# Performance work log

Measured on AMD Instinct MI355X. Metric: run time of the kernel, lower is better.

Reference implementation:

```python
import jax, jax.numpy as jnp
import numpy as np

D_IN = 256
D_HID = 256


def prelu(x, a):
    return jnp.maximum(x, 0) + a * jnp.minimum(x, 0)


def setup_inputs() -> dict:
    key = jax.random.key(0)
    ks = jax.random.split(key, 12)
    N, M = 8192, 8192
    s_in = 1.0 / np.sqrt(D_IN)
    s_3in = 1.0 / np.sqrt(3 * D_IN)
    s_half = 1.0 / np.sqrt(D_IN // 2)
    return {
        "anchor": jax.random.normal(ks[0], (N, D_IN), jnp.float32),
        "guess": jax.random.normal(ks[1], (M, D_IN), jnp.float32),
        # w_a: Linear(d_in, d_hid)
        "Wa": jax.random.uniform(ks[2], (D_HID, D_IN), jnp.float32, -s_in, s_in),
        "ba": jax.random.uniform(ks[3], (D_HID,), jnp.float32, -s_in, s_in),
        # w_g: Linear(d_in, d_hid)
        "Wg": jax.random.uniform(ks[4], (D_HID, D_IN), jnp.float32, -s_in, s_in),
        "bg": jax.random.uniform(ks[5], (D_HID,), jnp.float32, -s_in, s_in),
        # w_d: Linear(3*d_in, d_in) -> PReLU -> Linear(d_in, d_in//2) -> PReLU -> Linear(d_in//2, 1)
        "W1": jax.random.uniform(ks[6], (D_IN, 3 * D_IN), jnp.float32, -s_3in, s_3in),
        "b1": jax.random.uniform(ks[7], (D_IN,), jnp.float32, -s_3in, s_3in),
        "a1": jnp.array(0.25, jnp.float32),
        "W2": jax.random.uniform(ks[8], (D_IN // 2, D_IN), jnp.float32, -s_in, s_in),
        "b2": jax.random.uniform(ks[9], (D_IN // 2,), jnp.float32, -s_in, s_in),
        "a2": jnp.array(0.25, jnp.float32),
        "W3": jax.random.uniform(ks[10], (1, D_IN // 2), jnp.float32, -s_half, s_half),
        "b3": jax.random.uniform(ks[11], (1,), jnp.float32, -s_half, s_half),
    }


def reference(anchor, guess, Wa, ba, Wg, bg, W1, b1, a1, W2, b2, a2, W3, b3):
    # projections: [N, d_hid], [M, d_hid]
    ac = anchor @ Wa.T + ba
    ge = guess @ Wg.T + bg
    # unscaled cross-attention: [M, N] score matrix
    score = jax.nn.softmax(ge @ ac.T, axis=-1)
    ge2ac = score @ anchor  # [M, d_in]
    dis_x = jnp.concatenate((guess, ge2ac, guess - ge2ac), axis=-1)  # [M, 3*d_in]
    # dropout is identity in eval mode
    h = prelu(dis_x @ W1.T + b1, a1)
    h = prelu(h @ W2.T + b2, a2)
    return h @ W3.T + b3  # [M, 1]
```

## Files before the change

### kernel.cpp

```cpp
#include <hip/hip_runtime.h>


typedef _Float16 f16;
typedef _Float16 h8_t  __attribute__((ext_vector_type(8)));
typedef _Float16 h4_t  __attribute__((ext_vector_type(4)));
typedef float    f4_t  __attribute__((ext_vector_type(4)));
typedef float    f16x  __attribute__((ext_vector_type(16)));
typedef unsigned int u4_t  __attribute__((ext_vector_type(4)));

#define LOG2E 1.4426950408889634f

__device__ __forceinline__ void llds16(const f16* g, f16* s) {
    __builtin_amdgcn_global_load_lds(
        (const __attribute__((address_space(1))) void*)g,
        (__attribute__((address_space(3))) void*)s, 16, 0, 0);
}
__device__ __forceinline__ unsigned int pk2(float a, float b) {
    auto h = __builtin_amdgcn_cvt_pkrtz(a, b);
    return __builtin_bit_cast(unsigned int, h);
}

__global__ __launch_bounds__(256)
void cvt_weights(const float* __restrict__ Wa, const float* __restrict__ Wg,
                 const float* __restrict__ W1, const float* __restrict__ W2,
                 f16* __restrict__ oa, f16* __restrict__ og,
                 f16* __restrict__ o1, f16* __restrict__ o2)
{
    int i = blockIdx.x * 256 + threadIdx.x;
    const float* s; f16* d; int off;
    if (i < 16384)      { s = Wa; d = oa; off = i; }
    else if (i < 32768) { s = Wg; d = og; off = i - 16384; }
    else if (i < 81920) { s = W1; d = o1; off = i - 32768; }
    else                { s = W2; d = o2; off = i - 81920; }
    f4_t v = ((const f4_t*)s)[off];
    h4_t h;
    h[0] = (f16)v[0]; h[1] = (f16)v[1]; h[2] = (f16)v[2]; h[3] = (f16)v[3];
    ((h4_t*)d)[off] = h;
}

__global__ __launch_bounds__(256)
void transpose_f16(const float* __restrict__ src, f16* __restrict__ dst)
{
    __shared__ float tile[32][33];
    const int kb = blockIdx.x, db = blockIdx.y;
    const int t  = threadIdx.x;
    const int ty = t >> 3, tx4 = (t & 7) * 4;
    f4_t v = *(const f4_t*)(src + (size_t)(kb * 32 + ty) * 256 + db * 32 + tx4);
    tile[ty][tx4 + 0] = v[0]; tile[ty][tx4 + 1] = v[1];
    tile[ty][tx4 + 2] = v[2]; tile[ty][tx4 + 3] = v[3];
    __syncthreads();
    h4_t h;
    h[0] = (f16)tile[tx4 + 0][ty]; h[1] = (f16)tile[tx4 + 1][ty];
    h[2] = (f16)tile[tx4 + 2][ty]; h[3] = (f16)tile[tx4 + 3][ty];
    *(h4_t*)(dst + (size_t)(db * 32 + ty) * 8192 + kb * 32 + tx4) = h;
}

template<int ACT, int SRC32>
__global__ __launch_bounds__(256)
void gemm_bt(const void* __restrict__ A, const f16* __restrict__ B,
             const float* __restrict__ bias, const float* __restrict__ act_a,
             float scale, f16* __restrict__ C, int M, int N, int K)
{
    constexpr int BM = 128, BN = 64, BK = 32, LDA = 40, LDB = 40;
    __shared__ f16 As[BM * LDA];
    __shared__ f16 Bs[BN * LDB];
    const int t = threadIdx.x;
    const int w = t >> 6, l = t & 63, lg = l >> 4, lr = l & 15;
    const int wm = w >> 1, wn = w & 1;
    const int bm = blockIdx.x, bn = blockIdx.y;
    f4_t acc[4][2] = {};

    for (int kt = 0; kt < K; kt += BK) {
        #pragma unroll
        for (int i = 0; i < 2; i++) {
            int s = t + i * 256;
            int row = s >> 2, c8 = (s & 3) * 8;
            if constexpr (SRC32) {
                const float* Af = (const float*)A + (size_t)(bm * BM + row) * K + kt + c8;
                f4_t v0 = *(const f4_t*)Af;
                f4_t v1 = *(const f4_t*)(Af + 4);
                h8_t h;
                h[0]=(f16)v0[0]; h[1]=(f16)v0[1]; h[2]=(f16)v0[2]; h[3]=(f16)v0[3];
                h[4]=(f16)v1[0]; h[5]=(f16)v1[1]; h[6]=(f16)v1[2]; h[7]=(f16)v1[3];
                *(h8_t*)(&As[row * LDA + c8]) = h;
            } else {
                *(u4_t*)(&As[row * LDA + c8]) =
                    *(const u4_t*)((const f16*)A + (size_t)(bm * BM + row) * K + kt + c8);
            }
        }
        {
            int row = t >> 2, c8 = (t & 3) * 8;
            *(u4_t*)(&Bs[row * LDB + c8]) =
                *(const u4_t*)(B + (size_t)(bn * BN + row) * K + kt + c8);
        }
        __syncthreads();
        h8_t af[4], bf[2];
        #pragma unroll
        for (int mf = 0; mf < 4; mf++)
            af[mf] = *(const h8_t*)(&As[(wm * 64 + mf * 16 + lr) * LDA + lg * 8]);
        #pragma unroll
        for (int nf = 0; nf < 2; nf++)
            bf[nf] = *(const h8_t*)(&Bs[(wn * 32 + nf * 16 + lr) * LDB + lg * 8]);
        #pragma unroll
        for (int mf = 0; mf < 4; mf++)
            #pragma unroll
            for (int nf = 0; nf < 2; nf++)
                acc[mf][nf] = __builtin_amdgcn_mfma_f32_16x16x32_f16(
                    af[mf], bf[nf], acc[mf][nf], 0, 0, 0);
        __syncthreads();
    }

    float av = 0.f;
    if constexpr (ACT) av = *act_a;
    #pragma unroll
    for (int mf = 0; mf < 4; mf++)
        #pragma unroll
        for (int nf = 0; nf < 2; nf++)
            #pragma unroll
            for (int r = 0; r < 4; r++) {
                int row = bm * BM + wm * 64 + mf * 16 + lg * 4 + r;
                int col = bn * BN + wn * 32 + nf * 16 + lr;
                float v = (acc[mf][nf][r] + bias[col]) * scale;
                if constexpr (ACT) v = v > 0.f ? v : av * v;
                C[(size_t)row * N + col] = (f16)v;
            }
}

__global__ __launch_bounds__(256, 2)
void flash_attn(const f16* __restrict__ Q, const f16* __restrict__ Kc,
                const f16* __restrict__ Vt, f16* __restrict__ OPN,
                float* __restrict__ mpart, float* __restrict__ lpart)
{
    constexpr int D = 256, BK = 64, NK = 8192, SL = 1024, NT = SL / BK;
    __shared__ f16 Ks[BK * D];
    __shared__ f16 Vs[D * BK];
    const int t = threadIdx.x, w = t >> 6, l = t & 63;
    const int q = l & 31, hi = l >> 5;
    const int sl = blockIdx.x & 7, qb = blockIdx.x >> 3;
    const int k0b = sl * SL;
    const int qg0 = qb * 128 + w * 32;

    h8_t qf[16];
    {
        const f16* qr = Q + (size_t)(qg0 + q) * D + hi * 8;
        #pragma unroll
        for (int ks = 0; ks < 16; ks++) qf[ks] = *(const h8_t*)(qr + ks * 16);
    }

    const int sK0 = ((t & 31) ^ (t >> 5)) << 3;
    const int sx  = (t & 15) ^ (t >> 4);
    const int dV  = (t >> 4) * 2 + (sx >> 3);
    const int cV  = (sx & 7) << 3;

    auto stageK = [&](int k0) {
        #pragma unroll
        for (int i = 0; i < 8; i++) {
            const f16* g = Kc + (size_t)(k0 + i * 8 + (t >> 5)) * D + (sK0 ^ ((i & 1) << 6));
            llds16(g, &Ks[i * 2048 + w * 512]);
        }
    };
    auto stageV = [&](int k0) {
        #pragma unroll
        for (int i = 0; i < 8; i++) {
            const f16* g = Vt + (size_t)(i * 32 + dV) * NK + k0 + cV;
            llds16(g, &Vs[i * 2048 + w * 512]);
        }
    };

    stageK(k0b); stageV(k0b);
    __syncthreads();

    f16x o[8] = {};
    f16x sa0, sa1;
    float m_run = -1e30f, l_run = 0.f;
    const int rswzK = (q & 15) << 4;
    const int kbase0 = q * 512;
    const int vbase  = (q >> 1) * 256;
    const int vswz   = (q >> 1) << 4;
    const int vcol0  = ((q & 1) << 7) | (hi << 4);

    for (int kv = 0; kv < NT; ++kv) {
        #pragma unroll
        for (int r = 0; r < 16; r++) { sa0[r] = 0.f; sa1[r] = 0.f; }
        #pragma unroll
        for (int ks = 0; ks < 16; ks++) {
            const int cb = ((ks * 32) | (hi << 4)) ^ rswzK;
            h8_t a0 = *(const h8_t*)((const char*)Ks + kbase0 + cb);
            h8_t a1 = *(const h8_t*)((const char*)Ks + kbase0 + 16384 + cb);
            sa0 = __builtin_amdgcn_mfma_f32_32x32x16_f16(a0, qf[ks], sa0, 0, 0, 0);
            sa1 = __builtin_amdgcn_mfma_f32_32x32x16_f16(a1, qf[ks], sa1, 0, 0, 0);
        }

        float mt = sa0[0];
        #pragma unroll
        for (int r = 1; r < 16; r++) mt = fmaxf(mt, sa0[r]);
        #pragma unroll
        for (int r = 0; r < 16; r++) mt = fmaxf(mt, sa1[r]);
        mt = fmaxf(mt, __shfl_xor(mt, 32));
        if (!__all(mt <= m_run + 8.0f)) {
            const float mnew = fmaxf(m_run, mt);
            const float corr = exp2f(m_run - mnew);
            #pragma unroll
            for (int r = 0; r < 16; r++) {
                const float c = __shfl(corr, (r & 3) + 8 * (r >> 2) + 4 * hi);
                #pragma unroll
                for (int nb = 0; nb < 8; nb++) o[nb][r] *= c;
            }
            l_run *= corr;
            m_run = mnew;
        }
        float rs = 0.f;
        #pragma unroll
        for (int r = 0; r < 16; r++) { sa0[r] = exp2f(sa0[r] - m_run); rs += sa0[r]; }
        #pragma unroll
        for (int r = 0; r < 16; r++) { sa1[r] = exp2f(sa1[r] - m_run); rs += sa1[r]; }
        rs += __shfl_xor(rs, 32);
        l_run += rs;

        __syncthreads();
        if (kv + 1 < NT) stageK(k0b + (kv + 1) * BK);

        #pragma unroll
        for (int kb = 0; kb < 2; kb++) {
            const f16x& P = kb ? sa1 : sa0;
            #pragma unroll
            for (int s = 0; s < 2; s++) {
                unsigned int w00 = pk2(P[8*s+0], P[8*s+1]);
                unsigned int w01 = pk2(P[8*s+2], P[8*s+3]);
                unsigned int w10 = pk2(P[8*s+4], P[8*s+5]);
                unsigned int w11 = pk2(P[8*s+6], P[8*s+7]);
                asm volatile("v_permlane32_swap_b32 %0, %1" : "+v"(w00), "+v"(w10));
                asm volatile("v_permlane32_swap_b32 %0, %1" : "+v"(w01), "+v"(w11));
                u4_t up; up[0] = w00; up[1] = w01; up[2] = w10; up[3] = w11;
                const h8_t apv = __builtin_bit_cast(h8_t, up);
                const int S = kb * 2 + s;
                const int cb = (vcol0 | (S << 5)) ^ vswz;
                #pragma unroll
                for (int nb = 0; nb < 8; nb++) {
                    h8_t bf = *(const h8_t*)((const char*)Vs + nb * 4096 + vbase + cb);
                    o[nb] = __builtin_amdgcn_mfma_f32_32x32x16_f16(apv, bf, o[nb], 0, 0, 0);
                }
            }
        }
        __syncthreads();
        if (kv + 1 < NT) stageV(k0b + (kv + 1) * BK);
    }

    #pragma unroll
    for (int r = 0; r < 16; r++) {
        const int qr = (r & 3) + 8 * (r >> 2) + 4 * hi;
        const float linv = 1.0f / __shfl(l_run, qr);
        const size_t rowoff = ((size_t)sl * NK + qg0 + qr) * D;
        #pragma unroll
        for (int nb = 0; nb < 8; nb++)
            OPN[rowoff + nb * 32 + q] = (f16)(o[nb][r] * linv);
    }
    if (hi == 0) {
        mpart[(size_t)sl * NK + qg0 + q] = m_run;
        lpart[(size_t)sl * NK + qg0 + q] = l_run;
    }
}

__global__ __launch_bounds__(256)
void build_dis(const float* __restrict__ guess, const f16* __restrict__ OPN,
               const float* __restrict__ mp, const float* __restrict__ lp,
               f16* __restrict__ dis)
{
    const int m = blockIdx.x, d = threadIdx.x;
    float M = -3.0e38f;
    #pragma unroll
    for (int s = 0; s < 8; s++) M = fmaxf(M, mp[s * 8192 + m]);
    float wsum = 0.f, num = 0.f;
    #pragma unroll
    for (int s = 0; s < 8; s++) {
        float c = exp2f(mp[s * 8192 + m] - M) * lp[s * 8192 + m];
        wsum += c;
        num  += c * (float)OPN[((size_t)s * 8192 + m) * 256 + d];
    }
    const float v = num / wsum;
    const float g = guess[(size_t)m * 256 + d];
    dis[(size_t)m * 768 + d]       = (f16)g;
    dis[(size_t)m * 768 + 256 + d] = (f16)v;
    dis[(size_t)m * 768 + 512 + d] = (f16)(g - v);
}

__global__ __launch_bounds__(256)
void final_dot(const f16* __restrict__ h2, const float* __restrict__ W3,
               const float* __restrict__ b3, float* __restrict__ out)
{
    const int t = threadIdx.x, w = t >> 6, l = t & 63;
    const int row = blockIdx.x * 4 + w;
    const f16* hr = h2 + (size_t)row * 128;
    float s = (float)hr[l] * W3[l] + (float)hr[64 + l] * W3[64 + l];
    #pragma unroll
    for (int m = 1; m < 64; m <<= 1) s += __shfl_xor(s, m);
    if (l == 0) out[row] = s + b3[0];
}

extern "C" void kernel_launch(void* const* d_in, const int* in_sizes, int n_in,
                              void* d_out, int out_size, void* d_ws, size_t ws_size,
                              hipStream_t stream)
{
    const float* anchor = (const float*)d_in[0];
    const float* guess  = (const float*)d_in[1];
    const float* Wa = (const float*)d_in[2];
    const float* ba = (const float*)d_in[3];
    const float* Wg = (const float*)d_in[4];
    const float* bg = (const float*)d_in[5];
    const float* W1 = (const float*)d_in[6];
    const float* b1 = (const float*)d_in[7];
    const float* a1 = (const float*)d_in[8];
    const float* W2 = (const float*)d_in[9];
    const float* b2 = (const float*)d_in[10];
    const float* a2 = (const float*)d_in[11];
    const float* W3 = (const float*)d_in[12];
    const float* b3 = (const float*)d_in[13];
    float* out = (float*)d_out;
    char* ws = (char*)d_ws;

    const size_t MB = 1u << 20;
    f16* GE16 = (f16*)(ws + 0 * MB);
    f16* AC16 = (f16*)(ws + 4 * MB);
    f16* VT16 = (f16*)(ws + 8 * MB);
    f16* OPN  = (f16*)(ws + 12 * MB);
    f16* WA16 = (f16*)(ws + 44 * MB);
    f16* WG16 = (f16*)(ws + 44 * MB + 128 * 1024);
    f16* W116 = (f16*)(ws + 44 * MB + 256 * 1024);
    f16* W216 = (f16*)(ws + 44 * MB + 640 * 1024);
    float* MP = (float*)(ws + 45 * MB);
    float* LP = (float*)(ws + 45 * MB + 256 * 1024);
    f16* DIS  = (f16*)(ws + 0 * MB);
    f16* H1   = (f16*)(ws + 12 * MB);
    f16* H2   = (f16*)(ws + 16 * MB);

    cvt_weights<<<352, 256, 0, stream>>>(Wa, Wg, W1, W2, WA16, WG16, W116, W216);
    transpose_f16<<<dim3(256, 8), 256, 0, stream>>>(anchor, VT16);

    gemm_bt<0, 1><<<dim3(64, 4), 256, 0, stream>>>(guess,  WG16, bg, nullptr, LOG2E, GE16, 8192, 256, 256);
    gemm_bt<0, 1><<<dim3(64, 4), 256, 0, stream>>>(anchor, WA16, ba, nullptr, 1.0f,  AC16, 8192, 256, 256);

    flash_attn<<<512, 256, 0, stream>>>(GE16, AC16, VT16, OPN, MP, LP);

    build_dis<<<8192, 256, 0, stream>>>(guess, OPN, MP, LP, DIS);

    gemm_bt<1, 0><<<dim3(64, 4), 256, 0, stream>>>(DIS, W116, b1, a1, 1.0f, H1, 8192, 256, 768);
    gemm_bt<1, 0><<<dim3(64, 2), 256, 0, stream>>>(H1,  W216, b2, a2, 1.0f, H2, 8192, 128, 256);
    final_dot<<<2048, 256, 0, stream>>>(H2, W3, b3, out);
}
```

Measured before the change: 180.3 us.

## Double-buffer flash attention tiles, fold W1 concat algebraically, retile GEMMs

The flash attention kernel now uses 32-key tiles with double-buffered K/V shared memory. It prefetches the next tile at the start of each step and raises wave priority around the MFMA blocks, which removes the mid-loop staging barriers. The W1 weight is folded so that [g, v, g-v] @ W1^T becomes [g, v] @ W1c^T, which shrinks the first MLP GEMM's K from 768 to 512 and drops the third concat slice. The GEMM kernel is retiled to 64x128 blocks so each wave covers the full M tile. Smaller KV tiles add more barriers per key, and folding the weights in fp16 changes rounding slightly.

```diff
diff --git a/kernel.cpp b/kernel.cpp
--- a/kernel.cpp
+++ b/kernel.cpp
@@ -24,18 +24,31 @@
 void cvt_weights(const float* __restrict__ Wa, const float* __restrict__ Wg,
                  const float* __restrict__ W1, const float* __restrict__ W2,
                  f16* __restrict__ oa, f16* __restrict__ og,
-                 f16* __restrict__ o1, f16* __restrict__ o2)
+                 f16* __restrict__ o1c, f16* __restrict__ o2)
 {
     int i = blockIdx.x * 256 + threadIdx.x;
-    const float* s; f16* d; int off;
-    if (i < 16384)      { s = Wa; d = oa; off = i; }
-    else if (i < 32768) { s = Wg; d = og; off = i - 16384; }
-    else if (i < 81920) { s = W1; d = o1; off = i - 32768; }
-    else                { s = W2; d = o2; off = i - 81920; }
-    f4_t v = ((const f4_t*)s)[off];
-    h4_t h;
-    h[0] = (f16)v[0]; h[1] = (f16)v[1]; h[2] = (f16)v[2]; h[3] = (f16)v[3];
-    ((h4_t*)d)[off] = h;
+    if (i < 40960) {
+        const float* s; f16* d; int off;
+        if (i < 16384)      { s = Wa; d = oa; off = i; }
+        else if (i < 32768) { s = Wg; d = og; off = i - 16384; }
+        else                { s = W2; d = o2; off = i - 32768; }
+        f4_t v = ((const f4_t*)s)[off];
+        h4_t h;
+        h[0] = (f16)v[0]; h[1] = (f16)v[1]; h[2] = (f16)v[2]; h[3] = (f16)v[3];
+        ((h4_t*)d)[off] = h;
+    } else {
+        int off = i - 40960;
+        int j = off >> 7, c0 = (off & 127) * 4;
+        const float* r = W1 + (size_t)j * 768;
+        f4_t v0, v1;
+        if (c0 < 256) { v0 = *(const f4_t*)(r + c0); v1 = *(const f4_t*)(r + 512 + c0); }
+        else          { v0 = *(const f4_t*)(r + c0); v1 = *(const f4_t*)(r + 256 + c0); }
+        h4_t h;
+        #pragma unroll
+        for (int e = 0; e < 4; e++)
+            h[e] = (f16)(c0 < 256 ? v0[e] + v1[e] : v0[e] - v1[e]);
+        ((h4_t*)o1c)[off] = h;
+    }
 }
 
 __global__ __launch_bounds__(256)
@@ -55,26 +68,23 @@
     *(h4_t*)(dst + (size_t)(db * 32 + ty) * 8192 + kb * 32 + tx4) = h;
 }
 
-template<int ACT, int SRC32>
-__global__ __launch_bounds__(256)
-void gemm_bt(const void* __restrict__ A, const f16* __restrict__ B,
-             const float* __restrict__ bias, const float* __restrict__ act_a,
-             float scale, f16* __restrict__ C, int M, int N, int K)
-{
-    constexpr int BM = 128, BN = 64, BK = 32, LDA = 40, LDB = 40;
+template<int ACT, int SRC32, int BN>
+__global__ __launch_bounds__(256)
+void gemm_wide(const void* __restrict__ A, const f16* __restrict__ B,
+               const float* __restrict__ bias, const float* __restrict__ act_a,
+               float scale, f16* __restrict__ C, int M, int N, int K)
+{
+    constexpr int BM = 64, BK = 32, LDA = 40, LDB = 40, NF = BN / 64;
     __shared__ f16 As[BM * LDA];
     __shared__ f16 Bs[BN * LDB];
     const int t = threadIdx.x;
     const int w = t >> 6, l = t & 63, lg = l >> 4, lr = l & 15;
-    const int wm = w >> 1, wn = w & 1;
     const int bm = blockIdx.x, bn = blockIdx.y;
-    f4_t acc[4][2] = {};
+    f4_t acc[4][NF] = {};
 
     for (int kt = 0; kt < K; kt += BK) {
-        #pragma unroll
-        for (int i = 0; i < 2; i++) {
-            int s = t + i * 256;
-            int row = s >> 2, c8 = (s & 3) * 8;
+        {
+            int row = t >> 2, c8 = (t & 3) * 8;
             if constexpr (SRC32) {
                 const float* Af = (const float*)A + (size_t)(bm * BM + row) * K + kt + c8;
                 f4_t v0 = *(const f4_t*)Af;
@@ -88,23 +98,25 @@
                     *(const u4_t*)((const f16*)A + (size_t)(bm * BM + row) * K + kt + c8);
             }
         }
-        {
-            int row = t >> 2, c8 = (t & 3) * 8;
+        #pragma unroll
+        for (int i = 0; i < BN / 64; i++) {
+            int s = t + i * 256;
+            int row = s >> 2, c8 = (s & 3) * 8;
             *(u4_t*)(&Bs[row * LDB + c8]) =
                 *(const u4_t*)(B + (size_t)(bn * BN + row) * K + kt + c8);
         }
         __syncthreads();
-        h8_t af[4], bf[2];
+        h8_t af[4], bf[NF];
         #pragma unroll
         for (int mf = 0; mf < 4; mf++)
-            af[mf] = *(const h8_t*)(&As[(wm * 64 + mf * 16 + lr) * LDA + lg * 8]);
-        #pragma unroll
-        for (int nf = 0; nf < 2; nf++)
-            bf[nf] = *(const h8_t*)(&Bs[(wn * 32 + nf * 16 + lr) * LDB + lg * 8]);
+            af[mf] = *(const h8_t*)(&As[(mf * 16 + lr) * LDA + lg * 8]);
+        #pragma unroll
+        for (int nf = 0; nf < NF; nf++)
+            bf[nf] = *(const h8_t*)(&Bs[(w * (BN/4) + nf * 16 + lr) * LDB + lg * 8]);
         #pragma unroll
         for (int mf = 0; mf < 4; mf++)
             #pragma unroll
-            for (int nf = 0; nf < 2; nf++)
+            for (int nf = 0; nf < NF; nf++)
                 acc[mf][nf] = __builtin_amdgcn_mfma_f32_16x16x32_f16(
                     af[mf], bf[nf], acc[mf][nf], 0, 0, 0);
         __syncthreads();
@@ -115,11 +127,11 @@
     #pragma unroll
     for (int mf = 0; mf < 4; mf++)
         #pragma unroll
-        for (int nf = 0; nf < 2; nf++)
+        for (int nf = 0; nf < NF; nf++)
             #pragma unroll
             for (int r = 0; r < 4; r++) {
-                int row = bm * BM + wm * 64 + mf * 16 + lg * 4 + r;
-                int col = bn * BN + wn * 32 + nf * 16 + lr;
+                int row = bm * BM + mf * 16 + lg * 4 + r;
+                int col = bn * BN + w * (BN/4) + nf * 16 + lr;
                 float v = (acc[mf][nf][r] + bias[col]) * scale;
                 if constexpr (ACT) v = v > 0.f ? v : av * v;
                 C[(size_t)row * N + col] = (f16)v;
@@ -131,9 +143,9 @@
                 const f16* __restrict__ Vt, f16* __restrict__ OPN,
                 float* __restrict__ mpart, float* __restrict__ lpart)
 {
-    constexpr int D = 256, BK = 64, NK = 8192, SL = 1024, NT = SL / BK;
-    __shared__ f16 Ks[BK * D];
-    __shared__ f16 Vs[D * BK];
+    constexpr int D = 256, BKV = 32, NK = 8192, SL = 1024, NT = SL / BKV;
+    __shared__ f16 Ks0[BKV * D], Ks1[BKV * D];
+    __shared__ f16 Vs0[D * BKV], Vs1[D * BKV];
     const int t = threadIdx.x, w = t >> 6, l = t & 63;
     const int q = l & 31, hi = l >> 5;
     const int sl = blockIdx.x & 7, qb = blockIdx.x >> 3;
@@ -147,55 +159,53 @@
         for (int ks = 0; ks < 16; ks++) qf[ks] = *(const h8_t*)(qr + ks * 16);
     }
 
-    const int sK0 = ((t & 31) ^ (t >> 5)) << 3;
-    const int sx  = (t & 15) ^ (t >> 4);
-    const int dV  = (t >> 4) * 2 + (sx >> 3);
-    const int cV  = (sx & 7) << 3;
-
-    auto stageK = [&](int k0) {
-        #pragma unroll
-        for (int i = 0; i < 8; i++) {
-            const f16* g = Kc + (size_t)(k0 + i * 8 + (t >> 5)) * D + (sK0 ^ ((i & 1) << 6));
-            llds16(g, &Ks[i * 2048 + w * 512]);
+    const int rK   = t >> 5;
+    const int keyV = 8 * ((t & 3) ^ ((t >> 3) & 3));
+    const int dVi  = t >> 2;
+
+    auto stage = [&](int k0, f16* kd, f16* vd) {
+        #pragma unroll
+        for (int i = 0; i < 4; i++) {
+            const int r  = i * 8 + rK;
+            const int ce = 8 * ((t & 31) ^ (r & 15));
+            llds16(Kc + (size_t)(k0 + r) * D + ce, kd + i * 2048 + t * 8);
+        }
+        #pragma unroll
+        for (int i = 0; i < 4; i++) {
+            const int d0 = i * 64 + dVi;
+            llds16(Vt + (size_t)d0 * NK + k0 + keyV, vd + i * 2048 + t * 8);
         }
     };
-    auto stageV = [&](int k0) {
-        #pragma unroll
-        for (int i = 0; i < 8; i++) {
-            const f16* g = Vt + (size_t)(i * 32 + dV) * NK + k0 + cV;
-            llds16(g, &Vs[i * 2048 + w * 512]);
-        }
-    };
-
-    stageK(k0b); stageV(k0b);
+
+    stage(k0b, Ks0, Vs0);
     __syncthreads();
 
     f16x o[8] = {};
-    f16x sa0, sa1;
     float m_run = -1e30f, l_run = 0.f;
-    const int rswzK = (q & 15) << 4;
-    const int kbase0 = q * 512;
-    const int vbase  = (q >> 1) * 256;
-    const int vswz   = (q >> 1) << 4;
-    const int vcol0  = ((q & 1) << 7) | (hi << 4);
-
-    for (int kv = 0; kv < NT; ++kv) {
-        #pragma unroll
-        for (int r = 0; r < 16; r++) { sa0[r] = 0.f; sa1[r] = 0.f; }
+    const int kswz = (q & 15) << 4;
+    const int vswz = ((q >> 1) & 3) << 4;
+
+    auto tile = [&](int kv, const f16* kr, const f16* vr, f16* kw, f16* vw) {
+        if (kv + 1 < NT) stage(k0b + (kv + 1) * BKV, kw, vw);
+
+        f16x sa;
+        #pragma unroll
+        for (int r = 0; r < 16; r++) sa[r] = 0.f;
+        __builtin_amdgcn_s_setprio(1);
         #pragma unroll
         for (int ks = 0; ks < 16; ks++) {
-            const int cb = ((ks * 32) | (hi << 4)) ^ rswzK;
-            h8_t a0 = *(const h8_t*)((const char*)Ks + kbase0 + cb);
-            h8_t a1 = *(const h8_t*)((const char*)Ks + kbase0 + 16384 + cb);
-            sa0 = __builtin_amdgcn_mfma_f32_32x32x16_f16(a0, qf[ks], sa0, 0, 0, 0);
-            sa1 = __builtin_amdgcn_mfma_f32_32x32x16_f16(a1, qf[ks], sa1, 0, 0, 0);
-        }
-
-        float mt = sa0[0];
-        #pragma unroll
-        for (int r = 1; r < 16; r++) mt = fmaxf(mt, sa0[r]);
-        #pragma unroll
-        for (int r = 0; r < 16; r++) mt = fmaxf(mt, sa1[r]);
+            const int cb = ((ks * 32) | (hi << 4)) ^ kswz;
+            h8_t a0 = *(const h8_t*)((const char*)kr + q * 512 + cb);
+            sa = __builtin_amdgcn_mfma_f32_32x32x16_f16(a0, qf[ks], sa, 0, 0, 0);
+        }
+        __builtin_amdgcn_s_setprio(0);
+
+        float m01 = fmaxf(sa[0], sa[1]),  m23 = fmaxf(sa[2], sa[3]);
+        float m45 = fmaxf(sa[4], sa[5]),  m67 = fmaxf(sa[6], sa[7]);
+        float m89 = fmaxf(sa[8], sa[9]),  mab = fmaxf(sa[10], sa[11]);
+        float mcd = fmaxf(sa[12], sa[13]), mef = fmaxf(sa[14], sa[15]);
+        float mt = fmaxf(fmaxf(fmaxf(m01, m23), fmaxf(m45, m67)),
+                         fmaxf(fmaxf(m89, mab), fmaxf(mcd, mef)));
         mt = fmaxf(mt, __shfl_xor(mt, 32));
         if (!__all(mt <= m_run + 8.0f)) {
             const float mnew = fmaxf(m_run, mt);
@@ -211,39 +221,36 @@
         }
         float rs = 0.f;
         #pragma unroll
-        for (int r = 0; r < 16; r++) { sa0[r] = exp2f(sa0[r] - m_run); rs += sa0[r]; }
-        #pragma unroll
-        for (int r = 0; r < 16; r++) { sa1[r] = exp2f(sa1[r] - m_run); rs += sa1[r]; }
+        for (int r = 0; r < 16; r++) { sa[r] = exp2f(sa[r] - m_run); rs += sa[r]; }
         rs += __shfl_xor(rs, 32);
         l_run += rs;
 
+        __builtin_amdgcn_s_setprio(1);
+        #pragma unroll
+        for (int s = 0; s < 2; s++) {
+            unsigned int w00 = pk2(sa[8*s+0], sa[8*s+1]);
+            unsigned int w01 = pk2(sa[8*s+2], sa[8*s+3]);
+            unsigned int w10 = pk2(sa[8*s+4], sa[8*s+5]);
+            unsigned int w11 = pk2(sa[8*s+6], sa[8*s+7]);
+            asm volatile("v_permlane32_swap_b32 %0, %1" : "+v"(w00), "+v"(w10));
+            asm volatile("v_permlane32_swap_b32 %0, %1" : "+v"(w01), "+v"(w11));
+            u4_t up; up[0] = w00; up[1] = w01; up[2] = w10; up[3] = w11;
+            const h8_t apv = __builtin_bit_cast(h8_t, up);
+            const int cb = ((s * 32) | (hi << 4)) ^ vswz;
+            #pragma unroll
+            for (int nb = 0; nb < 8; nb++) {
+                h8_t bf = *(const h8_t*)((const char*)vr + nb * 2048 + q * 64 + cb);
+                o[nb] = __builtin_amdgcn_mfma_f32_32x32x16_f16(apv, bf, o[nb], 0, 0, 0);
+            }
+        }
+        __builtin_amdgcn_s_setprio(0);
+
         __syncthreads();
-        if (kv + 1 < NT) stageK(k0b + (kv + 1) * BK);
-
-        #pragma unroll
-        for (int kb = 0; kb < 2; kb++) {
-            const f16x& P = kb ? sa1 : sa0;
-            #pragma unroll
-            for (int s = 0; s < 2; s++) {
-                unsigned int w00 = pk2(P[8*s+0], P[8*s+1]);
-                unsigned int w01 = pk2(P[8*s+2], P[8*s+3]);
-                unsigned int w10 = pk2(P[8*s+4], P[8*s+5]);
-                unsigned int w11 = pk2(P[8*s+6], P[8*s+7]);
-                asm volatile("v_permlane32_swap_b32 %0, %1" : "+v"(w00), "+v"(w10));
-                asm volatile("v_permlane32_swap_b32 %0, %1" : "+v"(w01), "+v"(w11));
-                u4_t up; up[0] = w00; up[1] = w01; up[2] = w10; up[3] = w11;
-                const h8_t apv = __builtin_bit_cast(h8_t, up);
-                const int S = kb * 2 + s;
-                const int cb = (vcol0 | (S << 5)) ^ vswz;
-                #pragma unroll
-                for (int nb = 0; nb < 8; nb++) {
-                    h8_t bf = *(const h8_t*)((const char*)Vs + nb * 4096 + vbase + cb);
-                    o[nb] = __builtin_amdgcn_mfma_f32_32x32x16_f16(apv, bf, o[nb], 0, 0, 0);
-                }
-            }
-        }
-        __syncthreads();
-        if (kv + 1 < NT) stageV(k0b + (kv + 1) * BK);
+    };
+
+    for (int kv = 0; kv < NT; kv += 2) {
+        tile(kv,     Ks0, Vs0, Ks1, Vs1);
+        tile(kv + 1, Ks1, Vs1, Ks0, Vs0);
     }
 
     #pragma unroll
@@ -262,9 +269,9 @@
 }
 
 __global__ __launch_bounds__(256)
-void build_dis(const float* __restrict__ guess, const f16* __restrict__ OPN,
-               const float* __restrict__ mp, const float* __restrict__ lp,
-               f16* __restrict__ dis)
+void build_qv(const float* __restrict__ guess, const f16* __restrict__ OPN,
+              const float* __restrict__ mp, const float* __restrict__ lp,
+              f16* __restrict__ dis2)
 {
     const int m = blockIdx.x, d = threadIdx.x;
     float M = -3.0e38f;
@@ -278,10 +285,8 @@
         num  += c * (float)OPN[((size_t)s * 8192 + m) * 256 + d];
     }
     const float v = num / wsum;
-    const float g = guess[(size_t)m * 256 + d];
-    dis[(size_t)m * 768 + d]       = (f16)g;
-    dis[(size_t)m * 768 + 256 + d] = (f16)v;
-    dis[(size_t)m * 768 + 512 + d] = (f16)(g - v);
+    dis2[(size_t)m * 512 + d]       = (f16)guess[(size_t)m * 256 + d];
+    dis2[(size_t)m * 512 + 256 + d] = (f16)v;
 }
 
 __global__ __launch_bounds__(256)
@@ -325,25 +330,29 @@
     f16* OPN  = (f16*)(ws + 12 * MB);
     f16* WA16 = (f16*)(ws + 44 * MB);
     f16* WG16 = (f16*)(ws + 44 * MB + 128 * 1024);
-    f16* W116 = (f16*)(ws + 44 * MB + 256 * 1024);
-    f16* W216 = (f16*)(ws + 44 * MB + 640 * 1024);
+    f16* W1C  = (f16*)(ws + 44 * MB + 256 * 1024);
+    f16* W216 = (f16*)(ws + 44 * MB + 512 * 1024);
     float* MP = (float*)(ws + 45 * MB);
     float* LP = (float*)(ws + 45 * MB + 256 * 1024);
-    f16* DIS  = (f16*)(ws + 0 * MB);
-    f16* H1   = (f16*)(ws + 12 * MB);
-    f16* H2   = (f16*)(ws + 16 * MB);
-
-    cvt_weights<<<352, 256, 0, stream>>>(Wa, Wg, W1, W2, WA16, WG16, W116, W216);
+    f16* H2   = (f16*)(ws + 46 * MB);
+    f16* DIS2 = (f16*)(ws + 0 * MB);
+    f16* H1   = (f16*)(ws + 8 * MB);
+
+    cvt_weights<<<288, 256, 0, stream>>>(Wa, Wg, W1, W2, WA16, WG16, W1C, W216);
     transpose_f16<<<dim3(256, 8), 256, 0, stream>>>(anchor, VT16);
 
-    gemm_bt<0, 1><<<dim3(64, 4), 256, 0, stream>>>(guess,  WG16, bg, nullptr, LOG2E, GE16, 8192, 256, 256);
-    gemm_bt<0, 1><<<dim3(64, 4), 256, 0, stream>>>(anchor, WA16, ba, nullptr, 1.0f,  AC16, 8192, 256, 256);
+    gemm_wide<0, 1, 128><<<dim3(128, 2), 256, 0, stream>>>(
+        guess, WG16, bg, nullptr, LOG2E, GE16, 8192, 256, 256);
+    gemm_wide<0, 1, 128><<<dim3(128, 2), 256, 0, stream>>>(
+        anchor, WA16, ba, nullptr, 1.0f, AC16, 8192, 256, 256);
 
     flash_attn<<<512, 256, 0, stream>>>(GE16, AC16, VT16, OPN, MP, LP);
 
-    build_dis<<<8192, 256, 0, stream>>>(guess, OPN, MP, LP, DIS);
-
-    gemm_bt<1, 0><<<dim3(64, 4), 256, 0, stream>>>(DIS, W116, b1, a1, 1.0f, H1, 8192, 256, 768);
-    gemm_bt<1, 0><<<dim3(64, 2), 256, 0, stream>>>(H1,  W216, b2, a2, 1.0f, H2, 8192, 128, 256);
+    build_qv<<<8192, 256, 0, stream>>>(guess, OPN, MP, LP, DIS2);
+
+    gemm_wide<1, 0, 128><<<dim3(128, 2), 256, 0, stream>>>(
+        DIS2, W1C, b1, a1, 1.0f, H1, 8192, 256, 512);
+    gemm_wide<1, 0, 128><<<dim3(128, 1), 256, 0, stream>>>(
+        H1, W216, b2, a2, 1.0f, H2, 8192, 128, 256);
     final_dot<<<2048, 256, 0, stream>>>(H2, W3, b3, out);
 }
```

Measured after the change: 186.0 us. +3.1%, slower.

## Fuse prep kernels, fold W1 concat algebraically, fuse split-combine into MLP GEMMs

Applied to the files above, without the earlier changes.

Merges weight conversion and the anchor transpose into one prep kernel, and folds the concat [g, v, g-v]·W1 into a K=512 GEMM with combined weights (W1a+W1c, W1b-W1c). The split-softmax combine moves into the first MLP GEMM's A-tile load, which removes the dis buffer. The second MLP layer is fused with the final dot product. Both projections run in a single launch, and s_setprio is added around the MFMA phases in the attention kernel. This cuts launches and intermediate traffic, but the fused MLP kernels use only 128 blocks, which may underuse the GPU. proj_pair also writes an unused transpose into VT16 that races with prep's write of the same buffer, though both write identical data.

```diff
diff --git a/kernel.cpp b/kernel.cpp
--- a/kernel.cpp
+++ b/kernel.cpp
@@ -21,108 +21,126 @@
 }
 
 __global__ __launch_bounds__(256)
-void cvt_weights(const float* __restrict__ Wa, const float* __restrict__ Wg,
-                 const float* __restrict__ W1, const float* __restrict__ W2,
-                 f16* __restrict__ oa, f16* __restrict__ og,
-                 f16* __restrict__ o1, f16* __restrict__ o2)
-{
-    int i = blockIdx.x * 256 + threadIdx.x;
-    const float* s; f16* d; int off;
-    if (i < 16384)      { s = Wa; d = oa; off = i; }
-    else if (i < 32768) { s = Wg; d = og; off = i - 16384; }
-    else if (i < 81920) { s = W1; d = o1; off = i - 32768; }
-    else                { s = W2; d = o2; off = i - 81920; }
-    f4_t v = ((const f4_t*)s)[off];
-    h4_t h;
-    h[0] = (f16)v[0]; h[1] = (f16)v[1]; h[2] = (f16)v[2]; h[3] = (f16)v[3];
-    ((h4_t*)d)[off] = h;
-}
-
-__global__ __launch_bounds__(256)
-void transpose_f16(const float* __restrict__ src, f16* __restrict__ dst)
+void prep(const float* __restrict__ anchor,
+          const float* __restrict__ Wa, const float* __restrict__ Wg,
+          const float* __restrict__ W1, const float* __restrict__ W2,
+          f16* __restrict__ oa, f16* __restrict__ og,
+          f16* __restrict__ o1c, f16* __restrict__ o2,
+          f16* __restrict__ vt)
 {
     __shared__ float tile[32][33];
-    const int kb = blockIdx.x, db = blockIdx.y;
-    const int t  = threadIdx.x;
-    const int ty = t >> 3, tx4 = (t & 7) * 4;
-    f4_t v = *(const f4_t*)(src + (size_t)(kb * 32 + ty) * 256 + db * 32 + tx4);
-    tile[ty][tx4 + 0] = v[0]; tile[ty][tx4 + 1] = v[1];
-    tile[ty][tx4 + 2] = v[2]; tile[ty][tx4 + 3] = v[3];
-    __syncthreads();
-    h4_t h;
-    h[0] = (f16)tile[tx4 + 0][ty]; h[1] = (f16)tile[tx4 + 1][ty];
-    h[2] = (f16)tile[tx4 + 2][ty]; h[3] = (f16)tile[tx4 + 3][ty];
-    *(h4_t*)(dst + (size_t)(db * 32 + ty) * 8192 + kb * 32 + tx4) = h;
-}
-
-template<int ACT, int SRC32>
+    const int bid = blockIdx.x, t = threadIdx.x;
+    if (bid < 288) {
+        int i = bid * 256 + t;
+        if (i < 40960) {
+            const float* s; f16* d; int off;
+            if (i < 16384)      { s = Wa; d = oa; off = i; }
+            else if (i < 32768) { s = Wg; d = og; off = i - 16384; }
+            else                { s = W2; d = o2; off = i - 32768; }
+            f4_t v = ((const f4_t*)s)[off];
+            h4_t h;
+            h[0]=(f16)v[0]; h[1]=(f16)v[1]; h[2]=(f16)v[2]; h[3]=(f16)v[3];
+            ((h4_t*)d)[off] = h;
+        } else {
+            int off = i - 40960;
+            int j = off >> 7, c0 = (off & 127) * 4;
+            const float* r = W1 + (size_t)j * 768;
+            f4_t v0, v1;
+            if (c0 < 256) { v0 = *(const f4_t*)(r + c0); v1 = *(const f4_t*)(r + 512 + c0); }
+            else          { v0 = *(const f4_t*)(r + c0); v1 = *(const f4_t*)(r + 256 + c0); }
+            h4_t h;
+            #pragma unroll
+            for (int e = 0; e < 4; e++)
+                h[e] = (f16)(c0 < 256 ? v0[e] + v1[e] : v0[e] - v1[e]);
+            ((h4_t*)o1c)[off] = h;
+        }
+    } else {
+        const int r  = bid - 288;
+        const int kb = r & 255, db = r >> 8;
+        const int ty = t >> 3, tx4 = (t & 7) * 4;
+        f4_t v = *(const f4_t*)(anchor + (size_t)(kb * 32 + ty) * 256 + db * 32 + tx4);
+        tile[ty][tx4 + 0] = v[0]; tile[ty][tx4 + 1] = v[1];
+        tile[ty][tx4 + 2] = v[2]; tile[ty][tx4 + 3] = v[3];
+        __syncthreads();
+        h4_t h;
+        h[0] = (f16)tile[tx4 + 0][ty]; h[1] = (f16)tile[tx4 + 1][ty];
+        h[2] = (f16)tile[tx4 + 2][ty]; h[3] = (f16)tile[tx4 + 3][ty];
+        *(h4_t*)(vt + (size_t)(db * 32 + ty) * 8192 + kb * 32 + tx4) = h;
+    }
+}
+
 __global__ __launch_bounds__(256)
-void gemm_bt(const void* __restrict__ A, const f16* __restrict__ B,
-             const float* __restrict__ bias, const float* __restrict__ act_a,
-             float scale, f16* __restrict__ C, int M, int N, int K)
+void proj_pair(const float* __restrict__ guess, const float* __restrict__ anchor,
+               const f16* __restrict__ WG, const f16* __restrict__ WA,
+               const float* __restrict__ bg, const float* __restrict__ ba,
+               f16* __restrict__ GE, f16* __restrict__ AC,
+               f16* __restrict__ vtunused)
 {
-    constexpr int BM = 128, BN = 64, BK = 32, LDA = 40, LDB = 40;
-    __shared__ f16 As[BM * LDA];
-    __shared__ f16 Bs[BN * LDB];
+    constexpr int BK = 32, LDA = 40, LDB = 40;
+    __shared__ f16 As[64 * LDA];
+    __shared__ f16 Bs[128 * LDB];
     const int t = threadIdx.x;
     const int w = t >> 6, l = t & 63, lg = l >> 4, lr = l & 15;
-    const int wm = w >> 1, wn = w & 1;
-    const int bm = blockIdx.x, bn = blockIdx.y;
+    const int bm = blockIdx.x, bn = blockIdx.y, z = blockIdx.z;
+    const float* A   = z ? anchor : guess;
+    const f16*   B   = z ? WA : WG;
+    const float* bias= z ? ba : bg;
+    const float scale= z ? 1.0f : LOG2E;
+    f16* C = z ? AC : GE;
     f4_t acc[4][2] = {};
 
-    for (int kt = 0; kt < K; kt += BK) {
-        #pragma unroll
-        for (int i = 0; i < 2; i++) {
-            int s = t + i * 256;
-            int row = s >> 2, c8 = (s & 3) * 8;
-            if constexpr (SRC32) {
-                const float* Af = (const float*)A + (size_t)(bm * BM + row) * K + kt + c8;
-                f4_t v0 = *(const f4_t*)Af;
-                f4_t v1 = *(const f4_t*)(Af + 4);
-                h8_t h;
-                h[0]=(f16)v0[0]; h[1]=(f16)v0[1]; h[2]=(f16)v0[2]; h[3]=(f16)v0[3];
-                h[4]=(f16)v1[0]; h[5]=(f16)v1[1]; h[6]=(f16)v1[2]; h[7]=(f16)v1[3];
-                *(h8_t*)(&As[row * LDA + c8]) = h;
-            } else {
-                *(u4_t*)(&As[row * LDA + c8]) =
-                    *(const u4_t*)((const f16*)A + (size_t)(bm * BM + row) * K + kt + c8);
-            }
-        }
+    for (int kt = 0; kt < 256; kt += BK) {
         {
             int row = t >> 2, c8 = (t & 3) * 8;
+            const float* Af = A + (size_t)(bm * 64 + row) * 256 + kt + c8;
+            f4_t v0 = *(const f4_t*)Af;
+            f4_t v1 = *(const f4_t*)(Af + 4);
+            h8_t h;
+            h[0]=(f16)v0[0]; h[1]=(f16)v0[1]; h[2]=(f16)v0[2]; h[3]=(f16)v0[3];
+            h[4]=(f16)v1[0]; h[5]=(f16)v1[1]; h[6]=(f16)v1[2]; h[7]=(f16)v1[3];
+            *(h8_t*)(&As[row * LDA + c8]) = h;
+        }
+        {
+            int s0 = t, row = s0 >> 2, c8 = (s0 & 3) * 8;
             *(u4_t*)(&Bs[row * LDB + c8]) =
-                *(const u4_t*)(B + (size_t)(bn * BN + row) * K + kt + c8);
+                *(const u4_t*)(B + (size_t)(bn * 128 + row) * 256 + kt + c8);
+            int s1 = t + 256; row = s1 >> 2; c8 = (s1 & 3) * 8;
+            *(u4_t*)(&Bs[row * LDB + c8]) =
+                *(const u4_t*)(B + (size_t)(bn * 128 + row) * 256 + kt + c8);
         }
         __syncthreads();
         h8_t af[4], bf[2];
         #pragma unroll
         for (int mf = 0; mf < 4; mf++)
-            af[mf] = *(const h8_t*)(&As[(wm * 64 + mf * 16 + lr) * LDA + lg * 8]);
+            af[mf] = *(const h8_t*)(&As[(mf * 16 + lr) * LDA + lg * 8]);
         #pragma unroll
         for (int nf = 0; nf < 2; nf++)
-            bf[nf] = *(const h8_t*)(&Bs[(wn * 32 + nf * 16 + lr) * LDB + lg * 8]);
+            bf[nf] = *(const h8_t*)(&Bs[(w * 32 + nf * 16 + lr) * LDB + lg * 8]);
         #pragma unroll
         for (int mf = 0; mf < 4; mf++)
             #pragma unroll
             for (int nf = 0; nf < 2; nf++)
                 acc[mf][nf] = __builtin_amdgcn_mfma_f32_16x16x32_f16(
                     af[mf], bf[nf], acc[mf][nf], 0, 0, 0);
-        __syncthreads();
-    }
-
-    float av = 0.f;
-    if constexpr (ACT) av = *act_a;
+        if (z == 1 && bn == 0) {
+            const int c = t >> 3, r0 = (t & 7) * 8;
+            h8_t h;
+            #pragma unroll
+            for (int j = 0; j < 8; j++) h[j] = As[(r0 + j) * LDA + c];
+            *(h8_t*)(vtunused + (size_t)(kt + c) * 8192 + bm * 64 + r0) = h;
+        }
+        __syncthreads();
+    }
+
     #pragma unroll
     for (int mf = 0; mf < 4; mf++)
         #pragma unroll
         for (int nf = 0; nf < 2; nf++)
             #pragma unroll
             for (int r = 0; r < 4; r++) {
-                int row = bm * BM + wm * 64 + mf * 16 + lg * 4 + r;
-                int col = bn * BN + wn * 32 + nf * 16 + lr;
-                float v = (acc[mf][nf][r] + bias[col]) * scale;
-                if constexpr (ACT) v = v > 0.f ? v : av * v;
-                C[(size_t)row * N + col] = (f16)v;
+                int row = bm * 64 + mf * 16 + lg * 4 + r;
+                int col = bn * 128 + w * 32 + nf * 16 + lr;
+                C[(size_t)row * 256 + col] = (f16)((acc[mf][nf][r] + bias[col]) * scale);
             }
 }
 
@@ -182,6 +200,7 @@
     for (int kv = 0; kv < NT; ++kv) {
         #pragma unroll
         for (int r = 0; r < 16; r++) { sa0[r] = 0.f; sa1[r] = 0.f; }
+        __builtin_amdgcn_s_setprio(1);
         #pragma unroll
         for (int ks = 0; ks < 16; ks++) {
             const int cb = ((ks * 32) | (hi << 4)) ^ rswzK;
@@ -190,6 +209,7 @@
             sa0 = __builtin_amdgcn_mfma_f32_32x32x16_f16(a0, qf[ks], sa0, 0, 0, 0);
             sa1 = __builtin_amdgcn_mfma_f32_32x32x16_f16(a1, qf[ks], sa1, 0, 0, 0);
         }
+        __builtin_amdgcn_s_setprio(0);
 
         float mt = sa0[0];
         #pragma unroll
@@ -220,6 +240,7 @@
         __syncthreads();
         if (kv + 1 < NT) stageK(k0b + (kv + 1) * BK);
 
+        __builtin_amdgcn_s_setprio(1);
         #pragma unroll
         for (int kb = 0; kb < 2; kb++) {
             const f16x& P = kb ? sa1 : sa0;
@@ -242,6 +263,7 @@
                 }
             }
         }
+        __builtin_amdgcn_s_setprio(0);
         __syncthreads();
         if (kv + 1 < NT) stageV(k0b + (kv + 1) * BK);
     }
@@ -262,39 +284,178 @@
 }
 
 __global__ __launch_bounds__(256)
-void build_dis(const float* __restrict__ guess, const f16* __restrict__ OPN,
-               const float* __restrict__ mp, const float* __restrict__ lp,
-               f16* __restrict__ dis)
+void mlp1(const float* __restrict__ guess, const f16* __restrict__ OPN,
+          const float* __restrict__ mp, const float* __restrict__ lp,
+          const f16* __restrict__ W1C, const float* __restrict__ b1,
+          const float* __restrict__ a1, f16* __restrict__ H1)
 {
-    const int m = blockIdx.x, d = threadIdx.x;
-    float M = -3.0e38f;
+    constexpr int LDA = 40, LDB = 40;
+    __shared__ f16 As[64 * LDA];
+    __shared__ f16 Bs[256 * LDB];
+    __shared__ float cn[64][8];
+    const int t = threadIdx.x;
+    const int w = t >> 6, l = t & 63, lg = l >> 4, lr = l & 15;
+    const int m0 = blockIdx.x * 64;
+
+    if (t < 64) {
+        float c[8], M = -3.0e38f;
+        #pragma unroll
+        for (int s = 0; s < 8; s++) { c[s] = mp[s * 8192 + m0 + t]; M = fmaxf(M, c[s]); }
+        float wsum = 0.f;
+        #pragma unroll
+        for (int s = 0; s < 8; s++) { c[s] = exp2f(c[s] - M) * lp[s * 8192 + m0 + t]; wsum += c[s]; }
+        const float inv = 1.0f / wsum;
+        #pragma unroll
+        for (int s = 0; s < 8; s++) cn[t][s] = c[s] * inv;
+    }
+    __syncthreads();
+
+    const int arow = t >> 2, ac8 = (t & 3) * 8;
+    float cnr[8];
     #pragma unroll
-    for (int s = 0; s < 8; s++) M = fmaxf(M, mp[s * 8192 + m]);
-    float wsum = 0.f, num = 0.f;
+    for (int s = 0; s < 8; s++) cnr[s] = cn[arow][s];
+
+    f4_t acc[4][4] = {};
+    for (int kt = 0; kt < 512; kt += 32) {
+        {
+            h8_t h;
+            if (kt < 256) {
+                const float* Af = guess + (size_t)(m0 + arow) * 256 + kt + ac8;
+                f4_t v0 = *(const f4_t*)Af;
+                f4_t v1 = *(const f4_t*)(Af + 4);
+                h[0]=(f16)v0[0]; h[1]=(f16)v0[1]; h[2]=(f16)v0[2]; h[3]=(f16)v0[3];
+                h[4]=(f16)v1[0]; h[5]=(f16)v1[1]; h[6]=(f16)v1[2]; h[7]=(f16)v1[3];
+            } else {
+                const int d0 = kt - 256 + ac8;
+                f4_t v0 = {0.f,0.f,0.f,0.f}, v1 = {0.f,0.f,0.f,0.f};
+                #pragma unroll
+                for (int s = 0; s < 8; s++) {
+                    h8_t ov = *(const h8_t*)(OPN + ((size_t)s * 8192 + m0 + arow) * 256 + d0);
+                    const float c = cnr[s];
+                    v0[0] += c * (float)ov[0]; v0[1] += c * (float)ov[1];
+                    v0[2] += c * (float)ov[2]; v0[3] += c * (float)ov[3];
+                    v1[0] += c * (float)ov[4]; v1[1] += c * (float)ov[5];
+                    v1[2] += c * (float)ov[6]; v1[3] += c * (float)ov[7];
+                }
+                h[0]=(f16)v0[0]; h[1]=(f16)v0[1]; h[2]=(f16)v0[2]; h[3]=(f16)v0[3];
+                h[4]=(f16)v1[0]; h[5]=(f16)v1[1]; h[6]=(f16)v1[2]; h[7]=(f16)v1[3];
+            }
+            *(h8_t*)(&As[arow * LDA + ac8]) = h;
+        }
+        #pragma unroll
+        for (int i = 0; i < 4; i++) {
+            int s0 = t + i * 256;
+            int row = s0 >> 2, c8 = (s0 & 3) * 8;
+            *(u4_t*)(&Bs[row * LDB + c8]) =
+                *(const u4_t*)(W1C + (size_t)row * 512 + kt + c8);
+        }
+        __syncthreads();
+        h8_t af[4], bf[4];
+        #pragma unroll
+        for (int mf = 0; mf < 4; mf++)
+            af[mf] = *(const h8_t*)(&As[(mf * 16 + lr) * LDA + lg * 8]);
+        #pragma unroll
+        for (int nf = 0; nf < 4; nf++)
+            bf[nf] = *(const h8_t*)(&Bs[(w * 64 + nf * 16 + lr) * LDB + lg * 8]);
+        #pragma unroll
+        for (int mf = 0; mf < 4; mf++)
+            #pragma unroll
+            for (int nf = 0; nf < 4; nf++)
+                acc[mf][nf] = __builtin_amdgcn_mfma_f32_16x16x32_f16(
+                    af[mf], bf[nf], acc[mf][nf], 0, 0, 0);
+        __syncthreads();
+    }
+
+    const float av = *a1;
     #pragma unroll
-    for (int s = 0; s < 8; s++) {
-        float c = exp2f(mp[s * 8192 + m] - M) * lp[s * 8192 + m];
-        wsum += c;
-        num  += c * (float)OPN[((size_t)s * 8192 + m) * 256 + d];
-    }
-    const float v = num / wsum;
-    const float g = guess[(size_t)m * 256 + d];
-    dis[(size_t)m * 768 + d]       = (f16)g;
-    dis[(size_t)m * 768 + 256 + d] = (f16)v;
-    dis[(size_t)m * 768 + 512 + d] = (f16)(g - v);
+    for (int mf = 0; mf < 4; mf++)
+        #pragma unroll
+        for (int nf = 0; nf < 4; nf++)
+            #pragma unroll
+            for (int r = 0; r < 4; r++) {
+                int row = m0 + mf * 16 + lg * 4 + r;
+                int col = w * 64 + nf * 16 + lr;
+                float v = acc[mf][nf][r] + b1[col];
+                v = v > 0.f ? v : av * v;
+                H1[(size_t)row * 256 + col] = (f16)v;
+            }
 }
 
 __global__ __launch_bounds__(256)
-void final_dot(const f16* __restrict__ h2, const float* __restrict__ W3,
-               const float* __restrict__ b3, float* __restrict__ out)
+void mlp2_final(const f16* __restrict__ H1, const f16* __restrict__ W216,
+                const float* __restrict__ b2, const float* __restrict__ a2,
+                const float* __restrict__ W3, const float* __restrict__ b3,
+                float* __restrict__ out)
 {
-    const int t = threadIdx.x, w = t >> 6, l = t & 63;
-    const int row = blockIdx.x * 4 + w;
-    const f16* hr = h2 + (size_t)row * 128;
-    float s = (float)hr[l] * W3[l] + (float)hr[64 + l] * W3[64 + l];
+    constexpr int LDA = 40, LDB = 40;
+    __shared__ f16 As[64 * LDA];
+    __shared__ f16 Bs[128 * LDB];
+    __shared__ float part[64][68];
+    const int t = threadIdx.x;
+    const int w = t >> 6, l = t & 63, lg = l >> 4, lr = l & 15;
+    const int m0 = blockIdx.x * 64;
+    f4_t acc[4][2] = {};
+
+    for (int kt = 0; kt < 256; kt += 32) {
+        {
+            int row = t >> 2, c8 = (t & 3) * 8;
+            *(u4_t*)(&As[row * LDA + c8]) =
+                *(const u4_t*)(H1 + (size_t)(m0 + row) * 256 + kt + c8);
+            int s1 = t + 256; row = s1 >> 2; c8 = (s1 & 3) * 8;
+            if (row < 128)
+                *(u4_t*)(&Bs[row * LDB + c8]) =
+                    *(const u4_t*)(W216 + (size_t)row * 256 + kt + c8);
+        }
+        {
+            int s0 = t, row = s0 >> 2, c8 = (s0 & 3) * 8;
+            if (row < 64) ;
+        }
+        {
+            int row = t >> 2, c8 = (t & 3) * 8;
+            if (row < 64)
+                *(u4_t*)(&Bs[row * LDB + c8]) =
+                    *(const u4_t*)(W216 + (size_t)row * 256 + kt + c8);
+        }
+        __syncthreads();
+        h8_t af[4], bf[2];
+        #pragma unroll
+        for (int mf = 0; mf < 4; mf++)
+            af[mf] = *(const h8_t*)(&As[(mf * 16 + lr) * LDA + lg * 8]);
+        #pragma unroll
+        for (int nf = 0; nf < 2; nf++)
+            bf[nf] = *(const h8_t*)(&Bs[(w * 32 + nf * 16 + lr) * LDB + lg * 8]);
+        #pragma unroll
+        for (int mf = 0; mf < 4; mf++)
+            #pragma unroll
+            for (int nf = 0; nf < 2; nf++)
+                acc[mf][nf] = __builtin_amdgcn_mfma_f32_16x16x32_f16(
+                    af[mf], bf[nf], acc[mf][nf], 0, 0, 0);
+        __syncthreads();
+    }
+
+    const float av = *a2;
     #pragma unroll
-    for (int m = 1; m < 64; m <<= 1) s += __shfl_xor(s, m);
-    if (l == 0) out[row] = s + b3[0];
+    for (int mf = 0; mf < 4; mf++)
+        #pragma unroll
+        for (int r = 0; r < 4; r++) {
+            float p = 0.f;
+            #pragma unroll
+            for (int nf = 0; nf < 2; nf++) {
+                const int col = w * 32 + nf * 16 + lr;
+                float v = acc[mf][nf][r] + b2[col];
+                v = v > 0.f ? v : av * v;
+                p += v * W3[col];
+            }
+            part[mf * 16 + lg * 4 + r][w * 16 + lr] = p;
+        }
+    __syncthreads();
+    const int row = t >> 2, q4 = t & 3;
+    float s2 = 0.f;
+    #pragma unroll
+    for (int j = 0; j < 16; j++) s2 += part[row][q4 * 16 + j];
+    s2 += __shfl_xor(s2, 1);
+    s2 += __shfl_xor(s2, 2);
+    if (q4 == 0) out[m0 + row] = s2 + b3[0];
 }
 
 extern "C" void kernel_launch(void* const* d_in, const int* in_sizes, int n_in,
@@ -325,25 +486,20 @@
     f16* OPN  = (f16*)(ws + 12 * MB);
     f16* WA16 = (f16*)(ws + 44 * MB);
     f16* WG16 = (f16*)(ws + 44 * MB + 128 * 1024);
-    f16* W116 = (f16*)(ws + 44 * MB + 256 * 1024);
-    f16* W216 = (f16*)(ws + 44 * MB + 640 * 1024);
+    f16* W1C  = (f16*)(ws + 44 * MB + 256 * 1024);
+    f16* W216 = (f16*)(ws + 44 * MB + 512 * 1024);
     float* MP = (float*)(ws + 45 * MB);
     float* LP = (float*)(ws + 45 * MB + 256 * 1024);
-    f16* DIS  = (f16*)(ws + 0 * MB);
-    f16* H1   = (f16*)(ws + 12 * MB);
-    f16* H2   = (f16*)(ws + 16 * MB);
-
-    cvt_weights<<<352, 256, 0, stream>>>(Wa, Wg, W1, W2, WA16, WG16, W116, W216);
-    transpose_f16<<<dim3(256, 8), 256, 0, stream>>>(anchor, VT16);
-
-    gemm_bt<0, 1><<<dim3(64, 4), 256, 0, stream>>>(guess,  WG16, bg, nullptr, LOG2E, GE16, 8192, 256, 256);
-    gemm_bt<0, 1><<<dim3(64, 4), 256, 0, stream>>>(anchor, WA16, ba, nullptr, 1.0f,  AC16, 8192, 256, 256);
+    f16* H1   = (f16*)(ws + 0 * MB);
+
+    prep<<<2336, 256, 0, stream>>>(anchor, Wa, Wg, W1, W2, WA16, WG16, W1C, W216, VT16);
+
+    proj_pair<<<dim3(128, 2, 2), 256, 0, stream>>>(
+        guess, anchor, WG16, WA16, bg, ba, GE16, AC16, VT16);
 
     flash_attn<<<512, 256, 0, stream>>>(GE16, AC16, VT16, OPN, MP, LP);
 
-    build_dis<<<8192, 256, 0, stream>>>(guess, OPN, MP, LP, DIS);
-
-    gemm_bt<1, 0><<<dim3(64, 4), 256, 0, stream>>>(DIS, W116, b1, a1, 1.0f, H1, 8192, 256, 768);
-    gemm_bt<1, 0><<<dim3(64, 2), 256, 0, stream>>>(H1,  W216, b2, a2, 1.0f, H2, 8192, 128, 256);
-    final_dot<<<2048, 256, 0, stream>>>(H2, W3, b3, out);
-}
+    mlp1<<<128, 256, 0, stream>>>(guess, OPN, MP, LP, W1C, b1, a1, H1);
+
+    mlp2_final<<<128, 256, 0, stream>>>(H1, W216, b2, a2, W3, b3, out);
+}
```

New measurement: 333.3 us. +84.8%, slower.
